# Performance work log

Hardware: AMD Instinct MI355X
Metric: run time of the kernel (lower is better)

Reference implementation:

```python
import jax, jax.numpy as jnp
import numpy as np

B = 2048
NUM_GENES = 4096
# (stratum, n_terms, input_dim, output_dim, genes_per_term) leaves -> root
CFG = [(4, 256, 16, 20, 16), (3, 64, 144, 20, 64), (2, 16, 336, 77, 256), (1, 4, 1332, 308, 1024), (0, 1, 5328, 1229, 4096)]
EPS = 1e-5


def setup_inputs() -> dict:
    key = jax.random.key(0)
    ks = iter(jax.random.split(key, 64))
    inp = {"x": jax.random.uniform(next(ks), (B, NUM_GENES), dtype=jnp.float32)}
    sc = 0.05  # uniform init scale (original uses 0.001; scaled up for numerically robust baseline)
    for s, T, I, O, _ in CFG:
        inp[f"W{s}"] = jax.random.uniform(next(ks), (T, I, O), minval=-sc, maxval=sc, dtype=jnp.float32)
        inp[f"b{s}"] = jax.random.uniform(next(ks), (T, O), minval=-sc, maxval=sc, dtype=jnp.float32)
        inp[f"g{s}"] = jnp.ones((T, O), jnp.float32)   # BN weight
        inp[f"bb{s}"] = jnp.zeros((T, O), jnp.float32)  # BN bias
        inp[f"hw{s}"] = jax.random.uniform(next(ks), (T, O, 1), minval=-sc, maxval=sc, dtype=jnp.float32)
        inp[f"hb{s}"] = jnp.zeros((T, 1), jnp.float32)
    return inp


def _forward(x, W4, b4, g4, bb4, hw4, hb4, W3, b3, g3, bb3, hw3, hb3,
             W2, b2, g2, bb2, hw2, hb2, W1, b1, g1, bb1, hw1, hb1,
             W0, b0, g0, bb0, hw0, hb0):
    Bm = x.shape[0]
    params = [(W4, b4, g4, bb4, hw4, hb4), (W3, b3, g3, bb3, hw3, hb3),
              (W2, b2, g2, bb2, hw2, hb2), (W1, b1, g1, bb1, hw1, hb1),
              (W0, b0, g0, bb0, hw0, hb0)]
    act = None
    heads = []
    for (W, b, g, bb, hw, hb), (_, T, _, _, Gs) in zip(params, CFG):
        # gene states for each term: contiguous block gather == reshape
        genes = x.reshape(Bm, T, Gs)
        if act is None:
            inp = genes
        else:
            # concat 4 children outputs per parent, then gene states (children first, per _calculate_input_dim)
            inp = jnp.concatenate([act.reshape(Bm, T, -1), genes], axis=-1)
        # per-term Linear -> BatchNorm1d (training mode, biased var) -> Tanh, batched over terms
        h = jnp.einsum('bti,tio->bto', inp, W) + b
        mu = jnp.mean(h, axis=0)
        var = jnp.var(h, axis=0)
        act = jnp.tanh((h - mu) * jax.lax.rsqrt(var + EPS) * g + bb)
        # per-term linear head (output_size=1)
        heads.append(jnp.squeeze(jnp.einsum('bto,tos->bts', act, hw), -1) + hb[:, 0])
    # concat all per-term scalar outputs leaves->root; root prediction is heads[:, -1]
    return jnp.concatenate(heads, axis=1)


def reference(x, W4, b4, g4, bb4, hw4, hb4, W3, b3, g3, bb3, hw3, hb3,
              W2, b2, g2, bb2, hw2, hb2, W1, b1, g1, bb1, hw1, hb1,
              W0, b0, g0, bb0, hw0, hb0):
    return _forward(x, W4, b4, g4, bb4, hw4, hb4, W3, b3, g3, bb3, hw3, hb3,
                    W2, b2, g2, bb2, hw2, hb2, W1, b1, g1, bb1, hw1, hb1,
                    W0, b0, g0, bb0, hw0, hb0)
```

## Files before the change

kernel.cpp:

```cpp
#include <hip/hip_runtime.h>
#include <hip/hip_bf16.h>


#define BDIM 2048
#define OUTW 341

typedef __attribute__((ext_vector_type(8))) short short8;
typedef __attribute__((ext_vector_type(4))) float float4v;

static __device__ __forceinline__ unsigned short f2bf(float f) {
    union { float f; unsigned u; } c{f};
    unsigned r = c.u + 0x7FFF + ((c.u >> 16) & 1);
    return (unsigned short)(r >> 16);
}
static __device__ __forceinline__ float bf2f(unsigned short s) {
    union { unsigned u; float f; } c{(unsigned)s << 16};
    return c.f;
}

static __device__ __forceinline__ float fast_tanh(float x) {
    float ax = __builtin_fabsf(x);
    float e  = __builtin_amdgcn_exp2f(ax * 2.8853900817779268f);
    float r  = 1.f - 2.f * __builtin_amdgcn_rcpf(e + 1.f);
    return __builtin_copysignf(r, x);
}

static __device__ __forceinline__ void bn_ss(float sm, float sq, float g, float bb,
                                             float& scale, float& shift) {
    float mu = sm * (1.f / BDIM);
    float var = sq * (1.f / BDIM) - mu * mu;
    scale = rsqrtf(var + 1e-5f) * g;
    shift = bb - mu * scale;
}

static __device__ __forceinline__ void stage16(const void* g, void* ldsBase, int lane) {
#if __has_builtin(__builtin_amdgcn_global_load_lds)
    __builtin_amdgcn_global_load_lds(
        (const __attribute__((address_space(1))) unsigned int*)(uintptr_t)g,
        (__attribute__((address_space(3))) unsigned int*)(unsigned int)(uintptr_t)ldsBase,
        16, 0, 0);
#else
    *(uint4*)((char*)ldsBase + lane * 16) = *(const uint4*)g;
#endif
}

static __device__ __forceinline__ void cvt_w_body(const float* Wt, unsigned short* dst,
                                                  int I, int O, int Npad, int Kpad,
                                                  int i0, int o0, int tid) {
    __shared__ unsigned short tile[32][33];
    const int c = tid & 31, r0 = tid >> 5;
    #pragma unroll
    for (int rr = 0; rr < 4; rr++) {
        int i = i0 + r0 + rr * 8, o = o0 + c;
        float v = (i < I && o < O) ? Wt[(size_t)i * O + o] : 0.f;
        tile[r0 + rr * 8][c] = f2bf(v);
    }
    __syncthreads();
    #pragma unroll
    for (int rr = 0; rr < 4; rr++) {
        int o = o0 + r0 + rr * 8, k = i0 + c;
        if (o < Npad) dst[(size_t)o * Kpad + k] = tile[c][r0 + rr * 8];
    }
}

#define PACK_BLOCKS ((BDIM * 512 + BDIM * 24 + 255) / 256)
#define CVT_BLOCKS  2896
#define W0P1_BLOCKS (168 * 24)
__global__ __launch_bounds__(256) void pack_cvt(const float* __restrict__ x,
                                                unsigned short* __restrict__ ain0,
                                                unsigned short* __restrict__ ain1,
                                                const float* __restrict__ W4,
                                                const float* __restrict__ W3,
                                                const float* __restrict__ W2,
                                                const float* __restrict__ W1,
                                                const float* __restrict__ W0,
                                                unsigned short* __restrict__ wbt,
                                                float* __restrict__ acc) {
    int bid = blockIdx.x;
    if (bid < 20) {
        int idx = bid * 1024 + threadIdx.x * 4;
        *(float4*)(acc + idx) = make_float4(0.f, 0.f, 0.f, 0.f);
    }
    if (bid < PACK_BLOCKS) {
        const int MAIN = BDIM * 512;
        int i = bid * 256 + threadIdx.x;
        if (i < MAIN) {
            int b = i >> 9, j = i & 511;
            const float* xp = x + (size_t)b * 4096 + j * 8;
            float4 lo = *(const float4*)xp, hi = *(const float4*)(xp + 4);
            union { unsigned short u[8]; uint4 v4; uint2 v2[2]; } t;
            t.u[0] = f2bf(lo.x); t.u[1] = f2bf(lo.y); t.u[2] = f2bf(lo.z); t.u[3] = f2bf(lo.w);
            t.u[4] = f2bf(hi.x); t.u[5] = f2bf(hi.y); t.u[6] = f2bf(hi.z); t.u[7] = f2bf(hi.w);
            *(uint4*)(ain0 + (size_t)b * 5376 + 1232 + j * 8) = t.v4;
            int gi = j * 8, tt = gi >> 10, u = gi & 1023;
            unsigned short* d1 = ain1 + (size_t)b * 5376 + tt * 1344 + 308 + u;
            *(uint2*)d1 = t.v2[0];
            *(uint2*)(d1 + 4) = t.v2[1];
            return;
        }
        int zi = i - MAIN;
        const int ZU = BDIM * 12;
        if (zi < ZU) {
            int b = zi / 12, u = zi % 12;
            *(uint2*)(ain0 + (size_t)b * 5376 + 5328 + u * 4) = make_uint2(0u, 0u);
        } else if (zi < 2 * ZU) {
            zi -= ZU;
            int b = zi / 12, u = zi % 12, tt = u / 3, k = u % 3;
            *(uint2*)(ain1 + (size_t)b * 5376 + tt * 1344 + 1332 + k * 4) = make_uint2(0u, 0u);
        }
        return;
    }
    bid -= PACK_BLOCKS;
    if (bid >= CVT_BLOCKS) {
        bid -= CVT_BLOCKS;
        int bx = bid % 168, by = 16 + bid / 168;
        cvt_w_body(W0, wbt, 5328, 1229, 1280, 5376, bx * 32, by * 32, threadIdx.x);
        return;
    }
    const float* W; unsigned short* dst;
    int I, O, Npad, Kpad, gx, gy, local;
    if (bid < 256)       { W = W4; dst = wbt;           I = 16;   O = 20;  Npad = 20;  Kpad = 32;   gx = 1;  gy = 1;  local = bid; }
    else if (bid < 640)  { W = W3; dst = wbt + 163840;  I = 144;  O = 20;  Npad = 20;  Kpad = 192;  gx = 6;  gy = 1;  local = bid - 256; }
    else if (bid < 1216) { W = W2; dst = wbt + 409600;  I = 336;  O = 77;  Npad = 77;  Kpad = 384;  gx = 12; gy = 3;  local = bid - 640; }
    else                 { W = W1; dst = wbt + 882688;  I = 1332; O = 308; Npad = 320; Kpad = 1344; gx = 42; gy = 10; local = bid - 1216; }
    int per = gx * gy;
    int t = local / per, rem = local % per;
    int by = rem / gx, bx = rem % gx;
    cvt_w_body(W + (size_t)t * I * O, dst + (size_t)t * Npad * Kpad,
               I, O, Npad, Kpad, bx * 32, by * 32, threadIdx.x);
}

__global__ __launch_bounds__(256) void s4_stats(
    const unsigned short* __restrict__ xg,
    const unsigned short* __restrict__ wbt4,
    const float* __restrict__ b4,
    float* __restrict__ acc4)
{
    const int cg = blockIdx.x & 31;
    const int rc = blockIdx.x >> 5;
    const int t0 = cg * 8, b0 = rc * 64;
    const int tid = threadIdx.x;
    const int lane = tid & 63, w = tid >> 6;
    const int l15 = lane & 15, quad = lane >> 4;

    __shared__ __align__(16) unsigned short xs[64][168];

    #pragma unroll
    for (int j = 0; j < 4; j++) {
        int i = tid + j * 256;
        int r = i >> 4, gg = i & 15;
        *(uint4*)&xs[r][gg * 8] =
            *(const uint4*)(xg + (size_t)(b0 + r) * 5376 + t0 * 16 + gg * 8);
    }
    if (tid < 128) {
        int r = tid >> 1, gg = 16 + (tid & 1);
        *(uint4*)&xs[r][gg * 8] = make_uint4(0u, 0u, 0u, 0u);
    }
    __syncthreads();

    float4v acc[2][4][2];
    #pragma unroll
    for (int a = 0; a < 2; a++)
        #pragma unroll
        for (int b = 0; b < 4; b++)
            #pragma unroll
            for (int c = 0; c < 2; c++)
                acc[a][b][c] = (float4v){0.f, 0.f, 0.f, 0.f};

    #pragma unroll
    for (int ti = 0; ti < 2; ti++) {
        const int lt = w * 2 + ti;
        const int t = t0 + lt;
        short8 bf[2];
        #pragma unroll
        for (int nf = 0; nf < 2; nf++)
            bf[nf] = *(const short8*)(wbt4 + ((size_t)t * 20 + nf * 16 + l15) * 32 + quad * 8);
        #pragma unroll
        for (int mf = 0; mf < 4; mf++) {
            short8 a = *(const short8*)&xs[mf * 16 + l15][lt * 16 + quad * 8];
            #pragma unroll
            for (int nf = 0; nf < 2; nf++)
                acc[ti][mf][nf] = __builtin_amdgcn_mfma_f32_16x16x32_bf16(a, bf[nf], acc[ti][mf][nf], 0, 0, 0);
        }
    }

    #pragma unroll
    for (int ti = 0; ti < 2; ti++) {
        const int lt = w * 2 + ti;
        #pragma unroll
        for (int nf = 0; nf < 2; nf++) {
            const int o = nf * 16 + l15;
            const int col = (t0 + lt) * 20 + o;
            const bool valid = (o < 20);
            const float bias = valid ? b4[col] : 0.f;
            float s = 0.f, s2 = 0.f;
            #pragma unroll
            for (int mf = 0; mf < 4; mf++)
                #pragma unroll
                for (int r = 0; r < 4; r++) {
                    float v = acc[ti][mf][nf][r] + bias;
                    s += v; s2 += v * v;
                }
            s  += __shfl_xor(s, 16, 64);  s  += __shfl_xor(s, 32, 64);
            s2 += __shfl_xor(s2, 16, 64); s2 += __shfl_xor(s2, 32, 64);
            if (quad == 0 && valid) {
                atomicAdd(acc4 + col, s);
                atomicAdd(acc4 + 5120 + col, s2);
            }
        }
    }
}

__global__ __launch_bounds__(256) void s4s3_fused(
    const unsigned short* __restrict__ xg,
    const unsigned short* __restrict__ wbt4,
    const unsigned short* __restrict__ wbt3,
    const float* __restrict__ b4,
    const float* __restrict__ acc4,
    const float* __restrict__ g4,
    const float* __restrict__ bb4,
    const float* __restrict__ hw4,
    const float* __restrict__ hb4,
    const float* __restrict__ b3,
    unsigned short* __restrict__ h3,
    float* __restrict__ acc3,
    float* __restrict__ out)
{
    const int cg = blockIdx.x & 31;
    const int rc = blockIdx.x >> 5;
    const int t0 = cg * 8, b0 = rc * 64;
    const int tid = threadIdx.x;
    const int lane = tid & 63, w = tid >> 6;
    const int l15 = lane & 15, quad = lane >> 4;

    __shared__ __align__(16) unsigned short gs[64][152];
    __shared__ __align__(16) unsigned short as_[64][168];

    #pragma unroll
    for (int j = 0; j < 4; j++) {
        int i = tid + j * 256;
        int r = i >> 4, gg = i & 15;
        *(uint4*)&gs[r][gg * 8] =
            *(const uint4*)(xg + (size_t)(b0 + r) * 5376 + t0 * 16 + gg * 8);
    }
    if (tid < 128) {
        int r = tid >> 1, gg = 16 + (tid & 1);
        *(uint4*)&gs[r][gg * 8] = make_uint4(0u, 0u, 0u, 0u);
    }
    __syncthreads();

    float4v acc[2][4][2];
    #pragma unroll
    for (int a = 0; a < 2; a++)
        #pragma unroll
        for (int b = 0; b < 4; b++)
            #pragma unroll
            for (int c = 0; c < 2; c++)
                acc[a][b][c] = (float4v){0.f, 0.f, 0.f, 0.f};

    #pragma unroll
    for (int ti = 0; ti < 2; ti++) {
        const int lt = w * 2 + ti;
        const int t = t0 + lt;
        short8 bf[2];
        #pragma unroll
        for (int nf = 0; nf < 2; nf++)
            bf[nf] = *(const short8*)(wbt4 + ((size_t)t * 20 + nf * 16 + l15) * 32 + quad * 8);
        #pragma unroll
        for (int mf = 0; mf < 4; mf++) {
            short8 a = *(const short8*)&gs[mf * 16 + l15][lt * 16 + quad * 8];
            #pragma unroll
            for (int nf = 0; nf < 2; nf++)
                acc[ti][mf][nf] = __builtin_amdgcn_mfma_f32_16x16x32_bf16(a, bf[nf], acc[ti][mf][nf], 0, 0, 0);
        }
    }

    #pragma unroll
    for (int ti = 0; ti < 2; ti++) {
        const int lt = w * 2 + ti;
        const int t4 = t0 + lt;
        float hp[4][4];
        #pragma unroll
        for (int mf = 0; mf < 4; mf++)
            #pragma unroll
            for (int r = 0; r < 4; r++) hp[mf][r] = 0.f;
        #pragma unroll
        for (int nf = 0; nf < 2; nf++) {
            const int o = nf * 16 + l15;
            const int col = t4 * 20 + o;
            const bool valid = (o < 20);
            float scale = 0.f, shp = 0.f, hwv = 0.f;
            if (valid) {
                float sc, sh;
                bn_ss(acc4[col], acc4[5120 + col], g4[col], bb4[col], sc, sh);
                scale = sc;
                shp = b4[col] * sc + sh;
                hwv = hw4[col];
            }
            #pragma unroll
            for (int mf = 0; mf < 4; mf++)
                #pragma unroll
                for (int r = 0; r < 4; r++) {
                    float av = fast_tanh(acc[ti][mf][nf][r] * scale + shp);
                    if (valid)
                        as_[mf * 16 + quad * 4 + r][lt * 20 + o] = f2bf(av);
                    hp[mf][r] += av * hwv;
                }
        }
        const float hbv = hb4[t4];
        #pragma unroll
        for (int mf = 0; mf < 4; mf++)
            #pragma unroll
            for (int r = 0; r < 4; r++) {
                float v = hp[mf][r];
                v += __shfl_xor(v, 1, 64); v += __shfl_xor(v, 2, 64);
                v += __shfl_xor(v, 4, 64); v += __shfl_xor(v, 8, 64);
                if (l15 == 0)
                    out[(size_t)(b0 + mf * 16 + quad * 4 + r) * OUTW + t4] = v + hbv;
            }
    }
    __syncthreads();

    const int t3l = w & 1, mh = w >> 1;
    const int t3 = cg * 2 + t3l;
    float4v acc3r[2][2];
    #pragma unroll
    for (int a = 0; a < 2; a++)
        #pragma unroll
        for (int b = 0; b < 2; b++)
            acc3r[a][b] = (float4v){0.f, 0.f, 0.f, 0.f};

    #pragma unroll
    for (int ks = 0; ks < 5; ks++) {
        const int k = ks * 32 + quad * 8;
        short8 bf[2];
        #pragma unroll
        for (int nf = 0; nf < 2; nf++)
            bf[nf] = *(const short8*)(wbt3 + ((size_t)t3 * 20 + nf * 16 + l15) * 192 + ks * 32 + quad * 8);
        #pragma unroll
        for (int mf2 = 0; mf2 < 2; mf2++) {
            const int row = (mh * 2 + mf2) * 16 + l15;
            const unsigned short* ap = (k < 80) ? &as_[row][t3l * 80 + k]
                                                : &gs[row][t3l * 64 + (k - 80)];
            short8 a = *(const short8*)ap;
            #pragma unroll
            for (int nf = 0; nf < 2; nf++)
                acc3r[mf2][nf] = __builtin_amdgcn_mfma_f32_16x16x32_bf16(a, bf[nf], acc3r[mf2][nf], 0, 0, 0);
        }
    }

    float ss_[2], ss2_[2];
    #pragma unroll
    for (int nf = 0; nf < 2; nf++) { ss_[nf] = 0.f; ss2_[nf] = 0.f; }
    #pragma unroll
    for (int mf2 = 0; mf2 < 2; mf2++)
        #pragma unroll
        for (int nf = 0; nf < 2; nf++) {
            const int o = nf * 16 + l15;
            const int col = t3 * 20 + o;
            const bool valid = (o < 20);
            const float bias = valid ? b3[col] : 0.f;
            #pragma unroll
            for (int r = 0; r < 4; r++) {
                const int m = (mh * 2 + mf2) * 16 + quad * 4 + r;
                float v = acc3r[mf2][nf][r] + bias;
                if (valid)
                    h3[(size_t)(b0 + m) * 1280 + col] = f2bf(v);
                ss_[nf] += v; ss2_[nf] += v * v;
            }
        }
    #pragma unroll
    for (int nf = 0; nf < 2; nf++) {
        ss_[nf]  += __shfl_xor(ss_[nf], 16, 64);  ss_[nf]  += __shfl_xor(ss_[nf], 32, 64);
        ss2_[nf] += __shfl_xor(ss2_[nf], 16, 64); ss2_[nf] += __shfl_xor(ss2_[nf], 32, 64);
        const int o = nf * 16 + l15;
        if (quad == 0 && o < 20) {
            const int col = t3 * 20 + o;
            atomicAdd(acc3 + col, ss_[nf]);
            atomicAdd(acc3 + 1280 + col, ss2_[nf]);
        }
    }
}

__global__ __launch_bounds__(256) void s2_fused(
    const unsigned short* __restrict__ h3,
    const unsigned short* __restrict__ xg,
    const unsigned short* __restrict__ WbT,
    const float* __restrict__ acc3,
    const float* __restrict__ g3, const float* __restrict__ bb3,
    const float* __restrict__ hw3, const float* __restrict__ hb3,
    const float* __restrict__ b2,
    unsigned short* __restrict__ h,
    float* __restrict__ acc2,
    float* __restrict__ out)
{
    constexpr int BN = 96, BK = 64;
    constexpr int I = 336, O = 77, C = 80, Gs = 256, Kpad = 384;
    constexpr int hstride = 1232, TO = 1232;
    const int t  = blockIdx.z;
    const int b0 = blockIdx.y * 64;
    const int tid = threadIdx.x;
    const int lane = tid & 63;
    const int w = tid >> 6;
    const int l15 = lane & 15;
    const int quad = lane >> 4;

    constexpr int NF = BN / 32;
    const int wm = (w & 1) * 32;
    const int wn = (w >> 1) * (BN / 2);

    __shared__ __align__(16) unsigned short As[64][BK + 8];
    __shared__ __align__(16) unsigned short Bs[BN][BK + 8];
    __shared__ float ldsS[2][BN], ldsS2[2][BN];
    __shared__ float scL[80], shL[80], hwL[80];
    __shared__ float headAcc[64][4];

    if (tid < 80) {
        int col = t * 80 + tid;
        float sc, sh;
        bn_ss(acc3[col], acc3[1280 + col], g3[col], bb3[col], sc, sh);
        scL[tid] = sc; shL[tid] = sh; hwL[tid] = hw3[col];
    }
    headAcc[tid >> 2][tid & 3] = 0.f;
    __syncthreads();

    float4v accr[2][NF];
    #pragma unroll
    for (int a = 0; a < 2; a++)
        #pragma unroll
        for (int b = 0; b < NF; b++)
            accr[a][b] = (float4v){0.f, 0.f, 0.f, 0.f};

    constexpr int GR = BK / 8;
    constexpr int AG = 64 * GR;
    constexpr int BG = BN * GR;

    for (int k0 = 0; k0 < Kpad; k0 += BK) {
        #pragma unroll
        for (int g = tid; g < AG; g += 256) {
            const int r = g / GR, c8 = g % GR;
            const int k = k0 + c8 * 8;
            const int b = b0 + r;
            if (k + 8 <= C) {
                union { unsigned short u[8]; uint4 v; } hi_, ho;
                hi_.v = *(const uint4*)(h3 + (size_t)b * 1280 + t * 80 + k);
                const int tA = k / 20, tB = (k + 7) / 20;
                float pA = 0.f, pB = 0.f;
                #pragma unroll
                for (int j = 0; j < 8; j++) {
                    const int kk = k + j;
                    float av = fast_tanh(bf2f(hi_.u[j]) * scL[kk] + shL[kk]);
                    ho.u[j] = f2bf(av);
                    float pr = av * hwL[kk];
                    if (kk / 20 == tA) pA += pr; else pB += pr;
                }
                atomicAdd(&headAcc[r][tA], pA);
                if (tB != tA) atomicAdd(&headAcc[r][tB], pB);
                *(uint4*)&As[r][c8 * 8] = ho.v;
            } else if (k >= I) {
                *(uint4*)&As[r][c8 * 8] = make_uint4(0u, 0u, 0u, 0u);
            } else {
                *(uint4*)&As[r][c8 * 8] =
                    *(const uint4*)(xg + (size_t)b * 5376 + t * Gs + (k - C));
            }
        }
        #pragma unroll
        for (int g = tid; g < BG; g += 256) {
            const int n = g / GR, c8 = g % GR;
            uint4 v = make_uint4(0u, 0u, 0u, 0u);
            if (n < O)
                v = *(const uint4*)(WbT + ((size_t)t * O + n) * Kpad + k0 + c8 * 8);
            *(uint4*)&Bs[n][c8 * 8] = v;
        }
        __syncthreads();
        #pragma unroll
        for (int ks = 0; ks < BK / 32; ks++) {
            const int koff = ks * 32 + quad * 8;
            short8 a0 = *(const short8*)&As[wm + l15][koff];
            short8 a1 = *(const short8*)&As[wm + 16 + l15][koff];
            #pragma unroll
            for (int fn = 0; fn < NF; fn++) {
                short8 bf = *(const short8*)&Bs[wn + fn * 16 + l15][koff];
                accr[0][fn] = __builtin_amdgcn_mfma_f32_16x16x32_bf16(a0, bf, accr[0][fn], 0, 0, 0);
                accr[1][fn] = __builtin_amdgcn_mfma_f32_16x16x32_bf16(a1, bf, accr[1][fn], 0, 0, 0);
            }
        }
        __syncthreads();
    }

    {
        const int r = tid >> 2, t3l = tid & 3;
        const int t3 = t * 4 + t3l;
        out[(size_t)(b0 + r) * OUTW + 256 + t3] = headAcc[r][t3l] + hb3[t3];
    }

    float csum[NF], csum2[NF];
    #pragma unroll
    for (int fn = 0; fn < NF; fn++) { csum[fn] = 0.f; csum2[fn] = 0.f; }
    #pragma unroll
    for (int fm = 0; fm < 2; fm++)
        #pragma unroll
        for (int fn = 0; fn < NF; fn++)
            #pragma unroll
            for (int r = 0; r < 4; r++) {
                int m = wm + fm * 16 + quad * 4 + r;
                int o = wn + fn * 16 + l15;
                if (o < O) {
                    float v = accr[fm][fn][r] + b2[t * O + o];
                    h[(size_t)(b0 + m) * hstride + (size_t)t * O + o] = f2bf(v);
                    csum[fn] += v; csum2[fn] += v * v;
                }
            }
    #pragma unroll
    for (int fn = 0; fn < NF; fn++) {
        csum[fn]  += __shfl_xor(csum[fn], 16, 64);
        csum[fn]  += __shfl_xor(csum[fn], 32, 64);
        csum2[fn] += __shfl_xor(csum2[fn], 16, 64);
        csum2[fn] += __shfl_xor(csum2[fn], 32, 64);
    }
    if (quad == 0) {
        #pragma unroll
        for (int fn = 0; fn < NF; fn++) {
            ldsS[w & 1][wn + fn * 16 + l15]  = csum[fn];
            ldsS2[w & 1][wn + fn * 16 + l15] = csum2[fn];
        }
    }
    __syncthreads();
    if (tid < BN && tid < O) {
        int col = t * O + tid;
        atomicAdd(acc2 + col,      ldsS[0][tid] + ldsS[1][tid]);
        atomicAdd(acc2 + TO + col, ldsS2[0][tid] + ldsS2[1][tid]);
    }
}

template <int BN>
__global__ __launch_bounds__(256) void gemm_split(
    const unsigned short* __restrict__ A,
    const unsigned short* __restrict__ WbT,
    float* __restrict__ partial,
    int aStride, int tStride, int Kpad, int Npad, int KS, int TNpad,
    int nTiles, int TKS)
{
    const int tid = threadIdx.x;
    const int lane = tid & 63, w = tid >> 6;
    const int l15 = lane & 15, quad = lane >> 4;

    const int id = blockIdx.x;
    const int c = id & 7;
    const int tmp = id >> 3;
    const int n = tmp % nTiles;
    const int q = tmp / nTiles;
    const int group = q * 8 + c;
    const int b0 = (group / TKS) * 128;
    const int rem = group % TKS;
    const int t = rem / KS;
    const int ksIdx = rem - t * KS;
    const int n0 = n * BN;

    __shared__ __align__(16) unsigned short As[2][128 * 32];
    __shared__ __align__(16) unsigned short Bs[2][BN * 32];

    const int S = Kpad >> 5;
    const int qb = S / KS, rb = S % KS;
    const int beg = ksIdx * qb + (ksIdx < rb ? ksIdx : rb);
    const int cnt = qb + (ksIdx < rb ? 1 : 0);

    constexpr int NF = BN / 32;
    const int wm = (w & 1) * 64;
    const int wn = (w >> 1) * (BN / 2);

    float4v acc[4][NF];
    #pragma unroll
    for (int a = 0; a < 4; a++)
        #pragma unroll
        for (int b = 0; b < NF; b++)
            acc[a][b] = (float4v){0.f, 0.f, 0.f, 0.f};

    const unsigned short* aSrc[2];
    int aOff[2];
    #pragma unroll
    for (int j = 0; j < 2; j++) {
        int s = (w * 2 + j) * 64 + lane;
        int r = s >> 2, kg = (s & 3) ^ ((r >> 1) & 3);
        aSrc[j] = A + (size_t)(b0 + r) * aStride + (size_t)t * tStride + kg * 8;
        aOff[j] = (w * 2 + j) * 512;
    }
    constexpr int BCALLS = (BN == 128) ? 2 : 1;
    const unsigned short* bSrc[BCALLS];
    int bOff[BCALLS];
    #pragma unroll
    for (int j = 0; j < BCALLS; j++) {
        int s = (w * BCALLS + j) * 64 + lane;
        int r = s >> 2, kg = (s & 3) ^ ((r >> 1) & 3);
        bSrc[j] = WbT + ((size_t)t * Npad + n0 + r) * Kpad + kg * 8;
        bOff[j] = (w * BCALLS + j) * 512;
    }

    {
        const int k0 = beg << 5;
        #pragma unroll
        for (int j = 0; j < 2; j++)      stage16(aSrc[j] + k0, &As[0][aOff[j]], lane);
        #pragma unroll
        for (int j = 0; j < BCALLS; j++) stage16(bSrc[j] + k0, &Bs[0][bOff[j]], lane);
    }

    for (int s = 0; s < cnt; s++) {
        const int cur = s & 1;
        __syncthreads();
        if (s + 1 < cnt) {
            const int k1 = (beg + s + 1) << 5;
            #pragma unroll
            for (int j = 0; j < 2; j++)      stage16(aSrc[j] + k1, &As[cur ^ 1][aOff[j]], lane);
            #pragma unroll
            for (int j = 0; j < BCALLS; j++) stage16(bSrc[j] + k1, &Bs[cur ^ 1][bOff[j]], lane);
        }
        short8 af[4];
        #pragma unroll
        for (int fm = 0; fm < 4; fm++) {
            int m = wm + fm * 16 + l15;
            int pos = quad ^ ((m >> 1) & 3);
            af[fm] = *(const short8*)&As[cur][(m * 4 + pos) * 8];
        }
        short8 bfr[NF];
        #pragma unroll
        for (int fn = 0; fn < NF; fn++) {
            int nn = wn + fn * 16 + l15;
            int pos = quad ^ ((nn >> 1) & 3);
            bfr[fn] = *(const short8*)&Bs[cur][(nn * 4 + pos) * 8];
        }
        #pragma unroll
        for (int fm = 0; fm < 4; fm++)
            #pragma unroll
            for (int fn = 0; fn < NF; fn++)
                acc[fm][fn] = __builtin_amdgcn_mfma_f32_16x16x32_bf16(af[fm], bfr[fn], acc[fm][fn], 0, 0, 0);
    }

    const size_t pBase = ((size_t)ksIdx * BDIM + b0) * TNpad + (size_t)t * Npad + n0;
    #pragma unroll
    for (int fm = 0; fm < 4; fm++)
        #pragma unroll
        for (int r = 0; r < 4; r++) {
            const int m = wm + fm * 16 + quad * 4 + r;
            float* prow = partial + pBase + (size_t)m * TNpad + wn;
            #pragma unroll
            for (int fn = 0; fn < NF; fn++)
                prow[fn * 16 + l15] = acc[fm][fn][r];
        }
}

__global__ __launch_bounds__(256) void reduce1_cvtw0(
    const float* __restrict__ partial, const float* __restrict__ bias,
    unsigned short* __restrict__ h, float* __restrict__ acc,
    const float* __restrict__ W0, unsigned short* __restrict__ wbt)
{
    const int bid = blockIdx.x;
    if (bid >= 320) {
        int local = bid - 320;
        int bx = local % 168, by = local / 168;
        cvt_w_body(W0, wbt, 5328, 1229, 1280, 5376, bx * 32, by * 32, threadIdx.x);
        return;
    }
    constexpr int T = 4, O = 308, Npad = 320, KS = 2, hstride = 1232, TO = 1232;
    __shared__ float redS[4][64], redS2[4][64];
    const int colL = threadIdx.x & 63;
    const int cr = threadIdx.x >> 6;
    const int col = (bid % 20) * 64 + colL;
    const int chunk = bid / 20;
    float s = 0.f, s2 = 0.f;
    if (col < TO) {
        int t = col / O, o = col - t * O;
        const size_t TNpad = (size_t)T * Npad;
        const size_t pcol = (size_t)t * Npad + o;
        const float bv = bias[col];
        const int row0 = chunk * 128 + cr * 32;
        for (int r = 0; r < 32; r++) {
            const int row = row0 + r;
            const float* p = partial + (size_t)row * TNpad + pcol;
            float v = bv;
            for (int ks = 0; ks < KS; ks++) v += p[(size_t)ks * BDIM * TNpad];
            h[(size_t)row * hstride + col] = f2bf(v);
            s += v; s2 += v * v;
        }
    }
    redS[cr][colL] = s; redS2[cr][colL] = s2;
    __syncthreads();
    if (cr == 0 && col < TO) {
        float ts  = redS[0][colL] + redS[1][colL] + redS[2][colL] + redS[3][colL];
        float ts2 = redS2[0][colL] + redS2[1][colL] + redS2[2][colL] + redS2[3][colL];
        atomicAdd(acc + col, ts);
        atomicAdd(acc + TO + col, ts2);
    }
}

__global__ __launch_bounds__(256) void reduce_bias_stats(
    const float* __restrict__ partial, const float* __restrict__ bias,
    unsigned short* __restrict__ h, float* __restrict__ acc,
    int T, int O, int Npad, int KS, int hstride, int TO)
{
    __shared__ float redS[4][64], redS2[4][64];
    const int colL = threadIdx.x & 63;
    const int cr = threadIdx.x >> 6;
    const int col = blockIdx.x * 64 + colL;
    const int chunk = blockIdx.y;
    float s = 0.f, s2 = 0.f;
    if (col < TO) {
        int t = col / O, o = col - t * O;
        const size_t TNpad = (size_t)T * Npad;
        const size_t pcol = (size_t)t * Npad + o;
        const float bv = bias[col];
        const int row0 = chunk * 128 + cr * 32;
        for (int r = 0; r < 32; r++) {
            const int row = row0 + r;
            const float* p = partial + (size_t)row * TNpad + pcol;
            float v = bv;
            for (int ks = 0; ks < KS; ks++) v += p[(size_t)ks * BDIM * TNpad];
            h[(size_t)row * hstride + col] = f2bf(v);
            s += v; s2 += v * v;
        }
    }
    redS[cr][colL] = s; redS2[cr][colL] = s2;
    __syncthreads();
    if (cr == 0 && col < TO) {
        float ts  = redS[0][colL] + redS[1][colL] + redS[2][colL] + redS[3][colL];
        float ts2 = redS2[0][colL] + redS2[1][colL] + redS2[2][colL] + redS2[3][colL];
        atomicAdd(acc + col, ts);
        atomicAdd(acc + TO + col, ts2);
    }
}

__global__ __launch_bounds__(256) void bn_tanh_head(
    const unsigned short* __restrict__ h, const float* __restrict__ acc,
    const float* __restrict__ g, const float* __restrict__ bb,
    const float* __restrict__ hw, const float* __restrict__ hb,
    unsigned short* __restrict__ actOut, float* __restrict__ out,
    int T, int O, int hstride, int aRow, int GT, int GS, int head_off, int TO)
{
    int wid  = (blockIdx.x * 256 + threadIdx.x) >> 6;
    int lane = threadIdx.x & 63;
    int b = wid / T;
    int t = wid % T;
    const size_t hbase = (size_t)b * hstride + (size_t)t * O;
    const size_t abase = (size_t)b * aRow + (size_t)(t / GT) * GS + (size_t)(t % GT) * O;
    float hsum = 0.f;
    for (int o = lane; o < O; o += 64) {
        int col = t * O + o;
        float sc, sh;
        bn_ss(acc[col], acc[TO + col], g[col], bb[col], sc, sh);
        float a = fast_tanh(bf2f(h[hbase + o]) * sc + sh);
        if (actOut) actOut[abase + o] = f2bf(a);
        hsum += a * hw[col];
    }
    #pragma unroll
    for (int off = 32; off > 0; off >>= 1) hsum += __shfl_down(hsum, off, 64);
    if (lane == 0) out[(size_t)b * OUTW + head_off + t] = hsum + hb[t];
}

extern "C" void kernel_launch(void* const* d_in, const int* in_sizes, int n_in,
                              void* d_out, int out_size, void* d_ws, size_t ws_size,
                              hipStream_t stream)
{
    const float* x = (const float*)d_in[0];
    float* out = (float*)d_out;
    char* ws = (char*)d_ws;

    unsigned short* wbt  = (unsigned short*)(ws);
    unsigned short* ain0 = (unsigned short*)(ws + 13762560);
    unsigned short* bufB = (unsigned short*)(ws + 56754176);
    unsigned short* ain1 = (unsigned short*)(ws + 61997056);
    unsigned short* bufC = (unsigned short*)(ws + 84017152);
    float*          accB = (float*)(ws + 89063424);
    float* partial = (float*)(ws + 35782656);
    unsigned short* xg = ain0 + 1232;
    float* acc4 = accB;
    float* acc3 = accB + 10240;
    float* acc2 = accB + 12800;
    float* acc1 = accB + 15264;
    float* acc0 = accB + 17728;

    const float* W4 = (const float*)d_in[1];  const float* b4 = (const float*)d_in[2];
    const float* g4 = (const float*)d_in[3];  const float* bb4 = (const float*)d_in[4];
    const float* hw4 = (const float*)d_in[5]; const float* hb4 = (const float*)d_in[6];
    const float* W3 = (const float*)d_in[7];  const float* b3 = (const float*)d_in[8];
    const float* g3 = (const float*)d_in[9];  const float* bb3 = (const float*)d_in[10];
    const float* hw3 = (const float*)d_in[11]; const float* hb3 = (const float*)d_in[12];
    const float* W2 = (const float*)d_in[13]; const float* b2 = (const float*)d_in[14];
    const float* g2 = (const float*)d_in[15]; const float* bb2 = (const float*)d_in[16];
    const float* hw2 = (const float*)d_in[17]; const float* hb2 = (const float*)d_in[18];
    const float* W1 = (const float*)d_in[19]; const float* b1 = (const float*)d_in[20];
    const float* g1 = (const float*)d_in[21]; const float* bb1 = (const float*)d_in[22];
    const float* hw1 = (const float*)d_in[23]; const float* hb1 = (const float*)d_in[24];
    const float* W0 = (const float*)d_in[25]; const float* b0_ = (const float*)d_in[26];
    const float* g0 = (const float*)d_in[27]; const float* bb0 = (const float*)d_in[28];
    const float* hw0 = (const float*)d_in[29]; const float* hb0 = (const float*)d_in[30];

    pack_cvt<<<PACK_BLOCKS + CVT_BLOCKS + W0P1_BLOCKS, 256, 0, stream>>>(
        x, ain0, ain1, W4, W3, W2, W1, W0, wbt, accB);

    s4_stats<<<1024, 256, 0, stream>>>(xg, wbt, b4, acc4);
    s4s3_fused<<<1024, 256, 0, stream>>>(xg, wbt, wbt + 163840, b4, acc4, g4, bb4,
                                         hw4, hb4, b3, bufB, acc3, out);

    s2_fused<<<dim3(1, 32, 16), 256, 0, stream>>>(bufB, xg, wbt + 409600, acc3,
                                                  g3, bb3, hw3, hb3, b2,
                                                  bufC, acc2, out);
    bn_tanh_head<<<BDIM * 16 / 4, 256, 0, stream>>>(bufC, acc2, g2, bb2, hw2, hb2,
                                                    ain1, out, 16, 77, 1232, 5376, 4, 1344, 320, 1232);

    gemm_split<64><<<640, 256, 0, stream>>>(ain1, wbt + 882688, partial,
                                            5376, 1344, 1344, 320, 2, 1280, 5, 8);
    reduce1_cvtw0<<<320 + 2688, 256, 0, stream>>>(partial, b1, bufC, acc1, W0, wbt);
    bn_tanh_head<<<BDIM * 4 / 4, 256, 0, stream>>>(bufC, acc1, g1, bb1, hw1, hb1,
                                                   ain0, out, 4, 308, 1232, 5376, 4, 0, 336, 1232);

    gemm_split<128><<<640, 256, 0, stream>>>(ain0, wbt, partial,
                                             5376, 0, 5376, 1280, 4, 1280, 10, 4);
    reduce_bias_stats<<<dim3(20, 16), 256, 0, stream>>>(partial, b0_, bufC, acc0,
                                                        1, 1229, 1280, 4, 1232, 1229);
    bn_tanh_head<<<BDIM / 4, 256, 0, stream>>>(bufC, acc0, g0, bb0, hw0, hb0,
                                               nullptr, out, 1, 1229, 1232, 1232, 1, 0, 340, 1229);
}
```

Baseline: 372.7 us.

## Fuse BN-tanh-head of previous stratum into split-K GEMM A-tile staging

Removes two bn_tanh_head launches by applying batch-norm scale/shift and tanh to the raw pre-activation columns while staging the A tile inside the split-K GEMM (only for the k-split that covers those columns). The per-term head dot products are accumulated in shared memory by the n==0 tile and written to the output. This saves a full write and re-read of the activation buffer and two kernel launches. In exchange, the first k-split blocks do extra ALU work, and their loads for these columns become synchronous register loads instead of direct async staging, which adds load imbalance across splits and LDS atomics.

Measured after the change: 482.3 us. 29.4% more time.

```diff
diff --git a/kernel.cpp b/kernel.cpp
--- a/kernel.cpp
+++ b/kernel.cpp
@@ -533,14 +533,20 @@
     }
 }
 
-template <int BN>
-__global__ __launch_bounds__(256) void gemm_split(
+template <int BN, int ACTC>
+__global__ __launch_bounds__(256) void gemm_split_act(
     const unsigned short* __restrict__ A,
     const unsigned short* __restrict__ WbT,
     float* __restrict__ partial,
+    const unsigned short* __restrict__ hsrc,
+    const float* __restrict__ accS,
+    const float* __restrict__ gS, const float* __restrict__ bbS,
+    const float* __restrict__ hwS, const float* __restrict__ hbS,
+    float* __restrict__ out, int head_off,
     int aStride, int tStride, int Kpad, int Npad, int KS, int TNpad,
     int nTiles, int TKS)
 {
+    constexpr int CHILD = ACTC / 4;
     const int tid = threadIdx.x;
     const int lane = tid & 63, w = tid >> 6;
     const int l15 = lane & 15, quad = lane >> 4;
@@ -559,12 +565,27 @@
 
     __shared__ __align__(16) unsigned short As[2][128 * 32];
     __shared__ __align__(16) unsigned short Bs[2][BN * 32];
+    __shared__ float scS[ACTC], shS[ACTC], hwL[ACTC];
+    __shared__ float headAcc[128][4];
 
     const int S = Kpad >> 5;
     const int qb = S / KS, rb = S % KS;
     const int beg = ksIdx * qb + (ksIdx < rb ? ksIdx : rb);
     const int cnt = qb + (ksIdx < rb ? 1 : 0);
 
+    const bool doAct = (ksIdx == 0);
+    const bool isHead = doAct && (n == 0);
+    if (doAct) {
+        for (int cc = tid; cc < ACTC; cc += 256) {
+            int col = t * ACTC + cc;
+            float sc, sh;
+            bn_ss(accS[col], accS[1232 + col], gS[col], bbS[col], sc, sh);
+            scS[cc] = sc; shS[cc] = sh; hwL[cc] = hwS[col];
+        }
+        if (isHead)
+            for (int e = tid; e < 512; e += 256) headAcc[e >> 2][e & 3] = 0.f;
+    }
+
     constexpr int NF = BN / 32;
     const int wm = (w & 1) * 64;
     const int wn = (w >> 1) * (BN / 2);
@@ -577,12 +598,15 @@
             acc[a][b] = (float4v){0.f, 0.f, 0.f, 0.f};
 
     const unsigned short* aSrc[2];
-    int aOff[2];
+    const unsigned short* hRow[2];
+    int aOff[2], rA[2], kgA[2];
     #pragma unroll
     for (int j = 0; j < 2; j++) {
         int s = (w * 2 + j) * 64 + lane;
         int r = s >> 2, kg = (s & 3) ^ ((r >> 1) & 3);
+        rA[j] = r; kgA[j] = kg;
         aSrc[j] = A + (size_t)(b0 + r) * aStride + (size_t)t * tStride + kg * 8;
+        hRow[j] = hsrc + (size_t)(b0 + r) * 1232 + t * ACTC;
         aOff[j] = (w * 2 + j) * 512;
     }
     constexpr int BCALLS = (BN == 128) ? 2 : 1;
@@ -596,10 +620,48 @@
         bOff[j] = (w * BCALLS + j) * 512;
     }
 
+    auto xform = [&](int kcol, uint4 hvv, uint4 gvv, int rr, void* dst) {
+        union { unsigned short u[8]; uint4 v; } hi, gi, ho;
+        hi.v = hvv; gi.v = gvv;
+        float pA = 0.f, pB = 0.f;
+        const int cA = kcol / CHILD;
+        const int cB = (kcol + 7) / CHILD;
+        #pragma unroll
+        for (int e = 0; e < 8; e++) {
+            const int kk = kcol + e;
+            if (kk < ACTC) {
+                float av = fast_tanh(bf2f(hi.u[e]) * scS[kk] + shS[kk]);
+                ho.u[e] = f2bf(av);
+                if (isHead) {
+                    float pr = av * hwL[kk];
+                    if (kk / CHILD == cA) pA += pr; else pB += pr;
+                }
+            } else ho.u[e] = gi.u[e];
+        }
+        if (isHead && kcol < ACTC) {
+            atomicAdd(&headAcc[rr][cA], pA);
+            if (cB != cA && cB < 4) atomicAdd(&headAcc[rr][cB], pB);
+        }
+        *(uint4*)dst = ho.v;
+    };
+
+    __syncthreads();
+
     {
         const int k0 = beg << 5;
-        #pragma unroll
-        for (int j = 0; j < 2; j++)      stage16(aSrc[j] + k0, &As[0][aOff[j]], lane);
+        if (doAct && k0 < ACTC) {
+            #pragma unroll
+            for (int j = 0; j < 2; j++) {
+                const int kcol = k0 + kgA[j] * 8;
+                uint4 hvv = *(const uint4*)(hRow[j] + kcol);
+                uint4 gvv = (kcol + 8 > ACTC) ? *(const uint4*)(aSrc[j] + k0)
+                                              : make_uint4(0u, 0u, 0u, 0u);
+                xform(kcol, hvv, gvv, rA[j], &As[0][aOff[j] + lane * 8]);
+            }
+        } else {
+            #pragma unroll
+            for (int j = 0; j < 2; j++) stage16(aSrc[j] + k0, &As[0][aOff[j]], lane);
+        }
         #pragma unroll
         for (int j = 0; j < BCALLS; j++) stage16(bSrc[j] + k0, &Bs[0][bOff[j]], lane);
     }
@@ -607,10 +669,24 @@
     for (int s = 0; s < cnt; s++) {
         const int cur = s & 1;
         __syncthreads();
+        uint4 hv[2], gv[2];
+        bool nxtAct = false;
+        int k1 = 0;
         if (s + 1 < cnt) {
-            const int k1 = (beg + s + 1) << 5;
-            #pragma unroll
-            for (int j = 0; j < 2; j++)      stage16(aSrc[j] + k1, &As[cur ^ 1][aOff[j]], lane);
+            k1 = (beg + s + 1) << 5;
+            nxtAct = doAct && (k1 < ACTC);
+            if (nxtAct) {
+                #pragma unroll
+                for (int j = 0; j < 2; j++) {
+                    const int kcol = k1 + kgA[j] * 8;
+                    hv[j] = *(const uint4*)(hRow[j] + kcol);
+                    gv[j] = (kcol + 8 > ACTC) ? *(const uint4*)(aSrc[j] + k1)
+                                              : make_uint4(0u, 0u, 0u, 0u);
+                }
+            } else {
+                #pragma unroll
+                for (int j = 0; j < 2; j++)      stage16(aSrc[j] + k1, &As[cur ^ 1][aOff[j]], lane);
+            }
             #pragma unroll
             for (int j = 0; j < BCALLS; j++) stage16(bSrc[j] + k1, &Bs[cur ^ 1][bOff[j]], lane);
         }
@@ -633,6 +709,22 @@
             #pragma unroll
             for (int fn = 0; fn < NF; fn++)
                 acc[fm][fn] = __builtin_amdgcn_mfma_f32_16x16x32_bf16(af[fm], bfr[fn], acc[fm][fn], 0, 0, 0);
+        if (nxtAct) {
+            #pragma unroll
+            for (int j = 0; j < 2; j++) {
+                const int kcol = k1 + kgA[j] * 8;
+                xform(kcol, hv[j], gv[j], rA[j], &As[cur ^ 1][aOff[j] + lane * 8]);
+            }
+        }
+    }
+
+    __syncthreads();
+    if (isHead) {
+        for (int e = tid; e < 512; e += 256) {
+            int r = e >> 2, cc = e & 3;
+            out[(size_t)(b0 + r) * OUTW + head_off + t * 4 + cc] =
+                headAcc[r][cc] + hbS[t * 4 + cc];
+        }
     }
 
     const size_t pBase = ((size_t)ksIdx * BDIM + b0) * TNpad + (size_t)t * Npad + n0;
@@ -803,17 +895,17 @@
     s2_fused<<<dim3(1, 32, 16), 256, 0, stream>>>(bufB, xg, wbt + 409600, acc3,
                                                   g3, bb3, hw3, hb3, b2,
                                                   bufC, acc2, out);
-    bn_tanh_head<<<BDIM * 16 / 4, 256, 0, stream>>>(bufC, acc2, g2, bb2, hw2, hb2,
-                                                    ain1, out, 16, 77, 1232, 5376, 4, 1344, 320, 1232);
-
-    gemm_split<64><<<640, 256, 0, stream>>>(ain1, wbt + 882688, partial,
-                                            5376, 1344, 1344, 320, 2, 1280, 5, 8);
+
+    gemm_split_act<64, 308><<<640, 256, 0, stream>>>(
+        ain1, wbt + 882688, partial, bufC, acc2, g2, bb2, hw2, hb2, out, 320,
+        5376, 1344, 1344, 320, 2, 1280, 5, 8);
+
     reduce1_cvtw0<<<320 + 2688, 256, 0, stream>>>(partial, b1, bufC, acc1, W0, wbt);
-    bn_tanh_head<<<BDIM * 4 / 4, 256, 0, stream>>>(bufC, acc1, g1, bb1, hw1, hb1,
-                                                   ain0, out, 4, 308, 1232, 5376, 4, 0, 336, 1232);
-
-    gemm_split<128><<<640, 256, 0, stream>>>(ain0, wbt, partial,
-                                             5376, 0, 5376, 1280, 4, 1280, 10, 4);
+
+    gemm_split_act<128, 1232><<<640, 256, 0, stream>>>(
+        ain0, wbt, partial, bufC, acc1, g1, bb1, hw1, hb1, out, 336,
+        5376, 0, 5376, 1280, 4, 1280, 10, 4);
+
     reduce_bias_stats<<<dim3(20, 16), 256, 0, stream>>>(partial, b0_, bufC, acc0,
                                                         1, 1229, 1280, 4, 1232, 1229);
     bn_tanh_head<<<BDIM / 4, 256, 0, stream>>>(bufC, acc0, g0, bb0, hw0, hb0,
```
